# Performance work log

Hardware: AMD Instinct MI355X
Metric: run time of the kernel (lower is better)

Reference implementation:

```python
import jax, jax.numpy as jnp
import numpy as np

EMBED_DIM = 1024
NUM_HEADS = 16
HEAD_DIM = EMBED_DIM // NUM_HEADS


def setup_inputs() -> dict:
    key = jax.random.key(0)
    ks = jax.random.split(key, 6)
    B, S, D = 4, 2048, EMBED_DIM
    scale = 1.0 / np.sqrt(D)
    x = jax.random.normal(ks[0], (B, S, D), dtype=jnp.float32)
    mask = jnp.ones((B, S), dtype=jnp.int32)
    Wq = jax.random.normal(ks[1], (D, D), dtype=jnp.float32) * scale
    Wk = jax.random.normal(ks[2], (D, D), dtype=jnp.float32) * scale
    Wv = jax.random.normal(ks[3], (D, D), dtype=jnp.float32) * scale
    Wo = jax.random.normal(ks[4], (D, D), dtype=jnp.float32) * scale
    bq = jnp.zeros((D,), jnp.float32)
    bk = jnp.zeros((D,), jnp.float32)
    bv = jnp.zeros((D,), jnp.float32)
    bo = jnp.zeros((D,), jnp.float32)
    return {"x": x, "mask": mask, "Wq": Wq, "bq": bq, "Wk": Wk, "bk": bk,
            "Wv": Wv, "bv": bv, "Wo": Wo, "bo": bo}


def reference(x, mask, Wq, bq, Wk, bk, Wv, bv, Wo, bo):
    B, S, D = x.shape
    H, Hd = NUM_HEADS, HEAD_DIM

    def split_heads(t):  # [B,S,D] -> [B,H,S,Hd]
        return t.reshape(B, S, H, Hd).transpose(0, 2, 1, 3)

    q = split_heads(x @ Wq.T + bq)
    k = split_heads(x @ Wk.T + bk)
    v = split_heads(x @ Wv.T + bv)

    scores = jnp.einsum('bhqd,bhkd->bhqk', q, k) / jnp.sqrt(jnp.float32(Hd))
    # mask [B,S] -> broadcast over heads and query positions: [B,1,1,S]
    m = mask[:, None, None, :]
    scores = jnp.where(m == 0, jnp.float32(-1e9), scores)
    attn = jax.nn.softmax(scores, axis=-1)  # dropout_rate=0.0 (eval)
    out = jnp.einsum('bhqk,bhkd->bhqd', attn, v)
    out = out.transpose(0, 2, 1, 3).reshape(B, S, D)
    return out @ Wo.T + bo
```

## Files before the change

### kernel.cpp

```cpp
#include <hip/hip_runtime.h>
#include <stdint.h>

typedef __attribute__((ext_vector_type(8))) short short8;
typedef __attribute__((ext_vector_type(4))) float floatx4;
typedef __attribute__((ext_vector_type(16))) float f32x16;
typedef __attribute__((ext_vector_type(4))) unsigned int uint4v;

#define D_MODEL 1024
#define SEQ     2048
#define NHEAD   16
#define HDIM    64
#define BATCH   4
#define NW      (D_MODEL * D_MODEL)

__device__ __forceinline__ unsigned short f2b(float f) {
  unsigned int u = __builtin_bit_cast(unsigned int, f);
  u += 0x7FFFu + ((u >> 16) & 1u);
  return (unsigned short)(u >> 16);
}

__device__ __forceinline__ floatx4 mfma16(short8 a, short8 b, floatx4 c) {
  return __builtin_amdgcn_mfma_f32_16x16x32_bf16(a, b, c, 0, 0, 0);
}
__device__ __forceinline__ f32x16 mfma32(short8 a, short8 b, f32x16 c) {
  return __builtin_amdgcn_mfma_f32_32x32x16_bf16(a, b, c, 0, 0, 0);
}
__device__ __forceinline__ unsigned int cvtpk(float lo, float hi) {
  unsigned int r;
  asm("v_cvt_pk_bf16_f32 %0, %1, %2" : "=v"(r) : "v"(lo), "v"(hi));
  return r;
}
__device__ __forceinline__ void pl32swap(unsigned int &a, unsigned int &b) {
  asm("v_permlane32_swap_b32 %0, %1" : "+v"(a), "+v"(b));
}
__device__ __forceinline__ float expfast(float x) {
  return __builtin_amdgcn_exp2f(x);
}

#define GLL16(gsrc, ldst)                                                     \
  __builtin_amdgcn_global_load_lds(                                           \
      (const __attribute__((address_space(1))) void*)(gsrc),                  \
      (__attribute__((address_space(3))) void*)(ldst), 16, 0, 0)

__global__ void cvt_f32_bf16(const float* __restrict__ in,
                             unsigned short* __restrict__ out, int n) {
  int idx = (blockIdx.x * blockDim.x + threadIdx.x) * 4;
  int stride = gridDim.x * blockDim.x * 4;
  for (int i = idx; i < n; i += stride) {
    float4 v = *reinterpret_cast<const float4*>(in + i);
    ushort4 o;
    o.x = f2b(v.x); o.y = f2b(v.y); o.z = f2b(v.z); o.w = f2b(v.w);
    *reinterpret_cast<ushort4*>(out + i) = o;
  }
}

__global__ void cvt_w(const float* __restrict__ Wq, const float* __restrict__ Wk,
                      const float* __restrict__ Wv, const float* __restrict__ Wo,
                      unsigned short* __restrict__ Wqkv,
                      unsigned short* __restrict__ Wob,
                      const int* __restrict__ mask, float* __restrict__ maskb) {
  const int which = blockIdx.y;
  int idx = (blockIdx.x * blockDim.x + threadIdx.x) * 4;
  int stride = gridDim.x * blockDim.x * 4;
  if (which == 4) {
    for (int i = idx; i < BATCH * SEQ; i += stride) {
      int4 mv = *reinterpret_cast<const int4*>(mask + i);
      float4 o;
      o.x = mv.x ? 0.f : -1e10f;
      o.y = mv.y ? 0.f : -1e10f;
      o.z = mv.z ? 0.f : -1e10f;
      o.w = mv.w ? 0.f : -1e10f;
      *reinterpret_cast<float4*>(maskb + i) = o;
    }
    return;
  }
  const float* s = which == 0 ? Wq : which == 1 ? Wk : which == 2 ? Wv : Wo;
  unsigned short* d = which < 3 ? Wqkv + (size_t)which * NW : Wob;
  for (int i = idx; i < NW; i += stride) {
    float4 v = *reinterpret_cast<const float4*>(s + i);
    ushort4 o;
    o.x = f2b(v.x); o.y = f2b(v.y); o.z = f2b(v.z); o.w = f2b(v.w);
    *reinterpret_cast<ushort4*>(d + i) = o;
  }
}

__global__ void mask_flags(const int* __restrict__ mask,
                           unsigned int* __restrict__ flags2,
                           const float* __restrict__ bq,
                           const float* __restrict__ bk,
                           const float* __restrict__ bv,
                           float* __restrict__ bqkv) {
  const int b = blockIdx.x, tid = threadIdx.x;
  if (tid < 64) {
    int ok = 0;
    if (tid < 32) {
      ok = 1;
      for (int i = 0; i < 64; ++i) ok &= mask[b * SEQ + tid * 64 + i];
    }
    unsigned long long bal = __ballot(ok);
    if (tid == 0) flags2[b] = (unsigned int)bal;
  }
  const int i = blockIdx.x * 256 + tid;
  bqkv[i] = bq[i];
  bqkv[1024 + i] = bk[i];
  bqkv[2048 + i] = bv[i];
}

template <int MODE>
__global__ __launch_bounds__(256) void gemm_bt(
    const unsigned short* __restrict__ A, const unsigned short* __restrict__ B,
    const float* __restrict__ bias, void* __restrict__ C,
    unsigned short* __restrict__ VT, int M, int N, int K) {
  __shared__ __align__(16) unsigned short As[2][128 * 64];
  __shared__ __align__(16) unsigned short Bs[2][128 * 64];
  const int tid = threadIdx.x;
  const int w = tid >> 6, l = tid & 63, lg = l >> 4, li = l & 15;
  const int GX = (MODE == 1) ? 24 : 8;
  const int NWG = GX * 64;
  int id = blockIdx.y * GX + blockIdx.x;
  id = (id & 7) * (NWG >> 3) + (id >> 3);
  const int m0 = (id / GX) * 128, n0 = (id % GX) * 128;
  const int wr = w >> 1, wc = w & 1;

  floatx4 acc[4][4];
#pragma unroll
  for (int m = 0; m < 4; ++m)
#pragma unroll
    for (int n = 0; n < 4; ++n) acc[m][n] = (floatx4){0.f, 0.f, 0.f, 0.f};

#define GSTAGE(BUF, T)                                                         \
  do {                                                                         \
    _Pragma("unroll") for (int p = 0; p < 4; ++p) {                            \
      const int c = p * 256 + tid;                                             \
      const int row = c >> 3;                                                  \
      const int co = ((c & 7) ^ (row & 7)) * 8;                                \
      GLL16(A + (size_t)(m0 + row) * K + (T) * 64 + co,                        \
            &As[BUF][(p * 256 + w * 64) * 8]);                                 \
      GLL16(B + (size_t)(n0 + row) * K + (T) * 64 + co,                        \
            &Bs[BUF][(p * 256 + w * 64) * 8]);                                 \
    }                                                                          \
  } while (0)

#define GCOMP(BUF)                                                             \
  do {                                                                         \
    _Pragma("unroll") for (int kk = 0; kk < 2; ++kk) {                         \
      short8 af[4], bfr[4];                                                    \
      _Pragma("unroll") for (int m = 0; m < 4; ++m)                            \
        af[m] = *reinterpret_cast<const short8*>(                              \
            &As[BUF][(wr * 64 + m * 16 + li) * 64 +                            \
                     (((kk * 4 + lg) ^ (li & 7)) * 8)]);                       \
      _Pragma("unroll") for (int n = 0; n < 4; ++n)                            \
        bfr[n] = *reinterpret_cast<const short8*>(                             \
            &Bs[BUF][(wc * 64 + n * 16 + li) * 64 +                            \
                     (((kk * 4 + lg) ^ (li & 7)) * 8)]);                       \
      __builtin_amdgcn_s_setprio(1);                                           \
      _Pragma("unroll") for (int m = 0; m < 4; ++m)                            \
        _Pragma("unroll") for (int n = 0; n < 4; ++n)                          \
            acc[m][n] = mfma16(af[m], bfr[n], acc[m][n]);                      \
      __builtin_amdgcn_s_setprio(0);                                           \
    }                                                                          \
  } while (0)

  const int NT = K >> 6;
  GSTAGE(0, 0);
  __syncthreads();
#pragma unroll 1
  for (int t = 0; t < NT; t += 2) {
    if (t + 1 < NT) GSTAGE(1, t + 1);
    GCOMP(0);
    __syncthreads();
    if (t + 2 < NT) GSTAGE(0, t + 2);
    GCOMP(1);
    __syncthreads();
  }
#undef GSTAGE
#undef GCOMP

#pragma unroll
  for (int m = 0; m < 4; ++m)
#pragma unroll
    for (int n = 0; n < 4; ++n) {
      const int gcol = n0 + wc * 64 + n * 16 + li;
      const float bv = bias[gcol];
      const int grow0 = m0 + wr * 64 + m * 16 + lg * 4;
      if (MODE == 1 && n0 >= 2048) {
        const int vc = gcol - 2048;
        const int hh = vc >> 6, dd = vc & 63;
        const int b = grow0 >> 11, s0 = grow0 & 2047;
        ushort4 pk;
        pk.x = f2b(acc[m][n][0] + bv);
        pk.y = f2b(acc[m][n][1] + bv);
        pk.z = f2b(acc[m][n][2] + bv);
        pk.w = f2b(acc[m][n][3] + bv);
        *reinterpret_cast<ushort4*>(
            &VT[((size_t)((b * NHEAD + hh) * HDIM + dd)) * SEQ + s0]) = pk;
      } else {
        const float scl =
            (MODE == 1 && gcol < 1024) ? 0.18033688011112042f : 1.f;
#pragma unroll
        for (int r = 0; r < 4; ++r) {
          const float val = (acc[m][n][r] + bv) * scl;
          if (MODE == 2)
            reinterpret_cast<float*>(C)[(size_t)(grow0 + r) * N + gcol] = val;
          else
            reinterpret_cast<unsigned short*>(C)[(size_t)(grow0 + r) * N + gcol] =
                f2b(val);
        }
      }
    }
}

__global__ __launch_bounds__(512) void attn_v7(
    const unsigned short* __restrict__ QKV, const unsigned short* __restrict__ VT,
    const float* __restrict__ maskb, const unsigned int* __restrict__ flags2,
    unsigned short* __restrict__ O) {
  __shared__ __align__(16) unsigned short Kl[2][64 * 64];
  __shared__ __align__(16) unsigned short Vl[2][64 * 64];
  const int tid = threadIdx.x, w = tid >> 6, l = tid & 63;
  const int qi = l & 31, hi = l >> 5;
  const int bid = blockIdx.x;
  const int qblk = bid >> 6, bh = bid & 63, b = bh >> 4, h = bh & 15;
  const int q0 = qblk * 256 + w * 32;

  const unsigned short* qptr = QKV + (size_t)(b * SEQ + q0 + qi) * 3072 + h * 64;
  short8 qf[4];
#pragma unroll
  for (int ds = 0; ds < 4; ++ds)
    qf[ds] = *reinterpret_cast<const short8*>(qptr + ds * 16 + hi * 8);

  int off[2][4];
#pragma unroll
  for (int kb = 0; kb < 2; ++kb)
#pragma unroll
    for (int ds = 0; ds < 4; ++ds)
      off[kb][ds] = (kb * 32 + qi) * 64 + (((ds * 2 + hi) ^ (qi & 7)) * 8);

  const int srow = tid >> 3;
  const int swz = ((tid & 7) ^ (srow & 7)) * 8;
  const int ldst = w * 512;
  const unsigned short* kp0 =
      QKV + (size_t)(b * SEQ) * 3072 + D_MODEL + h * 64 + (size_t)srow * 3072 + swz;
  const unsigned short* vp0 =
      VT + (size_t)((b * NHEAD + h) * HDIM) * SEQ + (size_t)srow * SEQ + swz;

#define STAGE(BUF)                                                             \
  do {                                                                         \
    GLL16(kp0, &Kl[BUF][ldst]);                                                \
    GLL16(vp0, &Vl[BUF][ldst]);                                                \
    kp0 += 64 * 3072; vp0 += 64;                                               \
  } while (0)

  const float* mrow = maskb + b * SEQ;
  const unsigned int fl = flags2[b];
  f32x16 oa[2] = {};
  float l_run = 0.f;

#define TILE(BUF, KT)                                                          \
  do {                                                                         \
    f32x16 pa0 = {}, pa1 = {};                                                 \
    __builtin_amdgcn_s_setprio(1);                                             \
    _Pragma("unroll") for (int ds = 0; ds < 4; ++ds) {                         \
      const short8 kf0 =                                                       \
          *reinterpret_cast<const short8*>(&Kl[BUF][off[0][ds]]);              \
      const short8 kf1 =                                                       \
          *reinterpret_cast<const short8*>(&Kl[BUF][off[1][ds]]);              \
      pa0 = mfma32(kf0, qf[ds], pa0);                                          \
      pa1 = mfma32(kf1, qf[ds], pa1);                                          \
    }                                                                          \
    __builtin_amdgcn_s_setprio(0);                                             \
    if (!((fl >> (KT)) & 1)) {                \
      _Pragma("unroll") for (int rq = 0; rq < 4; ++rq) {                       \
        const float4 m0 = *reinterpret_cast<const float4*>(                    \
            mrow + (KT) * 64 + rq * 8 + hi * 4);                               \
        const float4 m1 = *reinterpret_cast<const float4*>(                    \
            mrow + (KT) * 64 + 32 + rq * 8 + hi * 4);                          \
        pa0[rq * 4 + 0] += m0.x; pa0[rq * 4 + 1] += m0.y;                      \
        pa0[rq * 4 + 2] += m0.z; pa0[rq * 4 + 3] += m0.w;                      \
        pa1[rq * 4 + 0] += m1.x; pa1[rq * 4 + 1] += m1.y;                      \
        pa1[rq * 4 + 2] += m1.z; pa1[rq * 4 + 3] += m1.w;                      \
      }                                                                        \
    }                                                                          \
    float r0 = 0.f, r1 = 0.f, r2 = 0.f, r3 = 0.f;                              \
    _Pragma("unroll") for (int r = 0; r < 16; r += 4) {                        \
      float p;                                                                 \
      p = expfast(pa0[r + 0]); pa0[r + 0] = p; r0 += p;                        \
      p = expfast(pa0[r + 1]); pa0[r + 1] = p; r1 += p;                        \
      p = expfast(pa0[r + 2]); pa0[r + 2] = p; r2 += p;                        \
      p = expfast(pa0[r + 3]); pa0[r + 3] = p; r3 += p;                        \
      p = expfast(pa1[r + 0]); pa1[r + 0] = p; r0 += p;                        \
      p = expfast(pa1[r + 1]); pa1[r + 1] = p; r1 += p;                        \
      p = expfast(pa1[r + 2]); pa1[r + 2] = p; r2 += p;                        \
      p = expfast(pa1[r + 3]); pa1[r + 3] = p; r3 += p;                        \
    }                                                                          \
    l_run += (r0 + r1) + (r2 + r3);                                            \
    unsigned int c0[8], c1[8];                                                 \
    _Pragma("unroll") for (int u2 = 0; u2 < 8; ++u2) {                         \
      c0[u2] = cvtpk(pa0[2 * u2], pa0[2 * u2 + 1]);                            \
      c1[u2] = cvtpk(pa1[2 * u2], pa1[2 * u2 + 1]);                            \
    }                                                                          \
    pl32swap(c0[0], c0[2]); pl32swap(c0[1], c0[3]);                            \
    pl32swap(c0[4], c0[6]); pl32swap(c0[5], c0[7]);                            \
    pl32swap(c1[0], c1[2]); pl32swap(c1[1], c1[3]);                            \
    pl32swap(c1[4], c1[6]); pl32swap(c1[5], c1[7]);                            \
    __builtin_amdgcn_s_setprio(1);                                             \
    _Pragma("unroll") for (int ks = 0; ks < 4; ++ks) {                         \
      const int kb = ks >> 1, hf = (ks & 1) * 4;                               \
      const short8 pf = __builtin_bit_cast(                                    \
          short8, kb ? (uint4v){c1[hf], c1[hf + 1], c1[hf + 2], c1[hf + 3]}    \
                     : (uint4v){c0[hf], c0[hf + 1], c0[hf + 2], c0[hf + 3]});  \
      const short8 vf0 =                                                       \
          *reinterpret_cast<const short8*>(&Vl[BUF][off[0][ks]]);              \
      const short8 vf1 =                                                       \
          *reinterpret_cast<const short8*>(&Vl[BUF][off[1][ks]]);              \
      oa[0] = mfma32(vf0, pf, oa[0]);                                          \
      oa[1] = mfma32(vf1, pf, oa[1]);                                          \
    }                                                                          \
    __builtin_amdgcn_s_setprio(0);                                             \
  } while (0)

  STAGE(0);
  __syncthreads();
#pragma unroll 1
  for (int kt = 0; kt < 32; kt += 2) {
    STAGE(1);
    TILE(0, kt);
    __syncthreads();
    if (kt + 2 < 32) STAGE(0);
    TILE(1, kt + 1);
    __syncthreads();
  }
#undef STAGE
#undef TILE

  l_run += __shfl_xor(l_run, 32);
  const float rinv = 1.f / l_run;
  unsigned int u[2][8];
#pragma unroll
  for (int vb = 0; vb < 2; ++vb) {
#pragma unroll
    for (int uu = 0; uu < 8; ++uu)
      u[vb][uu] = cvtpk(oa[vb][2 * uu] * rinv, oa[vb][2 * uu + 1] * rinv);
    pl32swap(u[vb][0], u[vb][2]);
    pl32swap(u[vb][1], u[vb][3]);
    pl32swap(u[vb][4], u[vb][6]);
    pl32swap(u[vb][5], u[vb][7]);
  }
  unsigned short* optr = O + (size_t)(b * SEQ + q0 + qi) * D_MODEL + h * 64;
#pragma unroll
  for (int cix = 0; cix < 4; ++cix) {
    const int vb = cix >> 1, hf = (cix & 1) * 4;
    *reinterpret_cast<short8*>(optr + cix * 16 + hi * 8) = __builtin_bit_cast(
        short8,
        (uint4v){u[vb][hf], u[vb][hf + 1], u[vb][hf + 2], u[vb][hf + 3]});
  }
}

extern "C" void kernel_launch(void* const* d_in, const int* in_sizes, int n_in,
                              void* d_out, int out_size, void* d_ws, size_t ws_size,
                              hipStream_t stream) {
  const float* x  = (const float*)d_in[0];
  const int* mask = (const int*)d_in[1];
  const float* Wq = (const float*)d_in[2];
  const float* bq = (const float*)d_in[3];
  const float* Wk = (const float*)d_in[4];
  const float* bk = (const float*)d_in[5];
  const float* Wv = (const float*)d_in[6];
  const float* bv = (const float*)d_in[7];
  const float* Wo = (const float*)d_in[8];
  const float* bo = (const float*)d_in[9];

  char* ws = (char*)d_ws;
  const size_t SZ_X = (size_t)BATCH * SEQ * D_MODEL * 2;
  unsigned short* xb    = (unsigned short*)(ws);
  unsigned short* Wqkvb = (unsigned short*)(ws + SZ_X);
  unsigned short* Wob   = (unsigned short*)(ws + SZ_X + 6u * 1024 * 1024);
  unsigned short* QKVb  = (unsigned short*)(ws + 24u * 1024 * 1024);
  unsigned short* VTb   = (unsigned short*)(ws + 72u * 1024 * 1024);
  float*          bqkv  = (float*)(ws + 88u * 1024 * 1024);
  float*          maskb = (float*)(ws + 88u * 1024 * 1024 + 16384);
  unsigned int*   flag2 = (unsigned int*)(ws + 88u * 1024 * 1024 + 49152);
  unsigned short* Ob    = xb;

  const int NX = BATCH * SEQ * D_MODEL;
  const int M = BATCH * SEQ;

  cvt_f32_bf16<<<2048, 256, 0, stream>>>(x, xb, NX);
  cvt_w<<<dim3(512, 5), 256, 0, stream>>>(Wq, Wk, Wv, Wo, Wqkvb, Wob, mask, maskb);
  mask_flags<<<BATCH, 256, 0, stream>>>(mask, flag2, bq, bk, bv, bqkv);

  gemm_bt<1><<<dim3(3 * D_MODEL / 128, M / 128), 256, 0, stream>>>(
      xb, Wqkvb, bqkv, QKVb, VTb, M, 3 * D_MODEL, D_MODEL);

  attn_v7<<<BATCH * NHEAD * (SEQ / 256), 512, 0, stream>>>(QKVb, VTb, maskb,
                                                           flag2, Ob);

  gemm_bt<2><<<dim3(D_MODEL / 128, M / 128), 256, 0, stream>>>(
      Ob, Wob, bo, d_out, nullptr, M, D_MODEL, D_MODEL);
}
```

Measured before the change: 185.5 us.

## Split attention KV range in two halves with persistent blocks and combine kernel

The attention kernel now splits each (batch, head, query-block) job into two halves over the key/value sequence. 768 persistent blocks loop over 1024 work items, and each writes unnormalized bf16 partial outputs plus row sums to scratch buffers. A new combine kernel adds the two partials and divides by the summed normalizer to produce the attention output. The aim is finer-grained work to improve load balance and CU utilisation, at the cost of an extra kernel launch, extra global traffic for the partials, and slight added rounding from storing the partials in bf16.

```diff
diff --git a/kernel.cpp b/kernel.cpp
--- a/kernel.cpp
+++ b/kernel.cpp
@@ -17,6 +17,9 @@
   unsigned int u = __builtin_bit_cast(unsigned int, f);
   u += 0x7FFFu + ((u >> 16) & 1u);
   return (unsigned short)(u >> 16);
+}
+__device__ __forceinline__ float b2f(unsigned short us) {
+  return __builtin_bit_cast(float, (unsigned int)us << 16);
 }
 
 __device__ __forceinline__ floatx4 mfma16(short8 a, short8 b, floatx4 c) {
@@ -210,149 +213,176 @@
     }
 }
 
-__global__ __launch_bounds__(512) void attn_v7(
+__global__ __launch_bounds__(512) void attn_v8(
     const unsigned short* __restrict__ QKV, const unsigned short* __restrict__ VT,
     const float* __restrict__ maskb, const unsigned int* __restrict__ flags2,
-    unsigned short* __restrict__ O) {
+    unsigned short* __restrict__ OP0, unsigned short* __restrict__ OP1,
+    float* __restrict__ l0g, float* __restrict__ l1g) {
   __shared__ __align__(16) unsigned short Kl[2][64 * 64];
   __shared__ __align__(16) unsigned short Vl[2][64 * 64];
   const int tid = threadIdx.x, w = tid >> 6, l = tid & 63;
   const int qi = l & 31, hi = l >> 5;
-  const int bid = blockIdx.x;
-  const int qblk = bid >> 6, bh = bid & 63, b = bh >> 4, h = bh & 15;
-  const int q0 = qblk * 256 + w * 32;
-
-  const unsigned short* qptr = QKV + (size_t)(b * SEQ + q0 + qi) * 3072 + h * 64;
-  short8 qf[4];
-#pragma unroll
-  for (int ds = 0; ds < 4; ++ds)
-    qf[ds] = *reinterpret_cast<const short8*>(qptr + ds * 16 + hi * 8);
-
-  int off[2][4];
-#pragma unroll
-  for (int kb = 0; kb < 2; ++kb)
+
+#pragma unroll 1
+  for (int item = blockIdx.x; item < 1024; item += 768) {
+    const int bh = item & 63, kvh = (item >> 6) & 1, qblk = item >> 7;
+    const int b = bh >> 4, h = bh & 15;
+    const int q0 = qblk * 256 + w * 32;
+
+    const unsigned short* qptr =
+        QKV + (size_t)(b * SEQ + q0 + qi) * 3072 + h * 64;
+    short8 qf[4];
 #pragma unroll
     for (int ds = 0; ds < 4; ++ds)
-      off[kb][ds] = (kb * 32 + qi) * 64 + (((ds * 2 + hi) ^ (qi & 7)) * 8);
-
-  const int srow = tid >> 3;
-  const int swz = ((tid & 7) ^ (srow & 7)) * 8;
-  const int ldst = w * 512;
-  const unsigned short* kp0 =
-      QKV + (size_t)(b * SEQ) * 3072 + D_MODEL + h * 64 + (size_t)srow * 3072 + swz;
-  const unsigned short* vp0 =
-      VT + (size_t)((b * NHEAD + h) * HDIM) * SEQ + (size_t)srow * SEQ + swz;
-
-#define STAGE(BUF)                                                             \
-  do {                                                                         \
-    GLL16(kp0, &Kl[BUF][ldst]);                                                \
-    GLL16(vp0, &Vl[BUF][ldst]);                                                \
-    kp0 += 64 * 3072; vp0 += 64;                                               \
+      qf[ds] = *reinterpret_cast<const short8*>(qptr + ds * 16 + hi * 8);
+
+    int off[2][4];
+#pragma unroll
+    for (int kb = 0; kb < 2; ++kb)
+#pragma unroll
+      for (int ds = 0; ds < 4; ++ds)
+        off[kb][ds] = (kb * 32 + qi) * 64 + (((ds * 2 + hi) ^ (qi & 7)) * 8);
+
+    const int srow = tid >> 3;
+    const int swz = ((tid & 7) ^ (srow & 7)) * 8;
+    const int ldst = w * 512;
+    const unsigned short* kp0 = QKV + (size_t)(b * SEQ) * 3072 + D_MODEL +
+                                h * 64 +
+                                (size_t)(kvh * 1024 + srow) * 3072 + swz;
+    const unsigned short* vp0 = VT + (size_t)((b * NHEAD + h) * HDIM) * SEQ +
+                                (size_t)srow * SEQ + kvh * 1024 + swz;
+
+#define STAGE(BUF)                                                            \
+  do {                                                                        \
+    GLL16(kp0, &Kl[BUF][ldst]);                                               \
+    GLL16(vp0, &Vl[BUF][ldst]);                                               \
+    kp0 += 64 * 3072; vp0 += 64;                                              \
   } while (0)
 
-  const float* mrow = maskb + b * SEQ;
-  const unsigned int fl = flags2[b];
-  f32x16 oa[2] = {};
-  float l_run = 0.f;
-
-#define TILE(BUF, KT)                                                          \
-  do {                                                                         \
-    f32x16 pa0 = {}, pa1 = {};                                                 \
-    __builtin_amdgcn_s_setprio(1);                                             \
-    _Pragma("unroll") for (int ds = 0; ds < 4; ++ds) {                         \
-      const short8 kf0 =                                                       \
-          *reinterpret_cast<const short8*>(&Kl[BUF][off[0][ds]]);              \
-      const short8 kf1 =                                                       \
-          *reinterpret_cast<const short8*>(&Kl[BUF][off[1][ds]]);              \
-      pa0 = mfma32(kf0, qf[ds], pa0);                                          \
-      pa1 = mfma32(kf1, qf[ds], pa1);                                          \
-    }                                                                          \
-    __builtin_amdgcn_s_setprio(0);                                             \
-    if (!((fl >> (KT)) & 1)) {                \
-      _Pragma("unroll") for (int rq = 0; rq < 4; ++rq) {                       \
-        const float4 m0 = *reinterpret_cast<const float4*>(                    \
-            mrow + (KT) * 64 + rq * 8 + hi * 4);                               \
-        const float4 m1 = *reinterpret_cast<const float4*>(                    \
-            mrow + (KT) * 64 + 32 + rq * 8 + hi * 4);                          \
-        pa0[rq * 4 + 0] += m0.x; pa0[rq * 4 + 1] += m0.y;                      \
-        pa0[rq * 4 + 2] += m0.z; pa0[rq * 4 + 3] += m0.w;                      \
-        pa1[rq * 4 + 0] += m1.x; pa1[rq * 4 + 1] += m1.y;                      \
-        pa1[rq * 4 + 2] += m1.z; pa1[rq * 4 + 3] += m1.w;                      \
-      }                                                                        \
-    }                                                                          \
-    float r0 = 0.f, r1 = 0.f, r2 = 0.f, r3 = 0.f;                              \
-    _Pragma("unroll") for (int r = 0; r < 16; r += 4) {                        \
-      float p;                                                                 \
-      p = expfast(pa0[r + 0]); pa0[r + 0] = p; r0 += p;                        \
-      p = expfast(pa0[r + 1]); pa0[r + 1] = p; r1 += p;                        \
-      p = expfast(pa0[r + 2]); pa0[r + 2] = p; r2 += p;                        \
-      p = expfast(pa0[r + 3]); pa0[r + 3] = p; r3 += p;                        \
-      p = expfast(pa1[r + 0]); pa1[r + 0] = p; r0 += p;                        \
-      p = expfast(pa1[r + 1]); pa1[r + 1] = p; r1 += p;                        \
-      p = expfast(pa1[r + 2]); pa1[r + 2] = p; r2 += p;                        \
-      p = expfast(pa1[r + 3]); pa1[r + 3] = p; r3 += p;                        \
-    }                                                                          \
-    l_run += (r0 + r1) + (r2 + r3);                                            \
-    unsigned int c0[8], c1[8];                                                 \
-    _Pragma("unroll") for (int u2 = 0; u2 < 8; ++u2) {                         \
-      c0[u2] = cvtpk(pa0[2 * u2], pa0[2 * u2 + 1]);                            \
-      c1[u2] = cvtpk(pa1[2 * u2], pa1[2 * u2 + 1]);                            \
-    }                                                                          \
-    pl32swap(c0[0], c0[2]); pl32swap(c0[1], c0[3]);                            \
-    pl32swap(c0[4], c0[6]); pl32swap(c0[5], c0[7]);                            \
-    pl32swap(c1[0], c1[2]); pl32swap(c1[1], c1[3]);                            \
-    pl32swap(c1[4], c1[6]); pl32swap(c1[5], c1[7]);                            \
-    __builtin_amdgcn_s_setprio(1);                                             \
-    _Pragma("unroll") for (int ks = 0; ks < 4; ++ks) {                         \
-      const int kb = ks >> 1, hf = (ks & 1) * 4;                               \
-      const short8 pf = __builtin_bit_cast(                                    \
-          short8, kb ? (uint4v){c1[hf], c1[hf + 1], c1[hf + 2], c1[hf + 3]}    \
-                     : (uint4v){c0[hf], c0[hf + 1], c0[hf + 2], c0[hf + 3]});  \
-      const short8 vf0 =                                                       \
-          *reinterpret_cast<const short8*>(&Vl[BUF][off[0][ks]]);              \
-      const short8 vf1 =                                                       \
-          *reinterpret_cast<const short8*>(&Vl[BUF][off[1][ks]]);              \
-      oa[0] = mfma32(vf0, pf, oa[0]);                                          \
-      oa[1] = mfma32(vf1, pf, oa[1]);                                          \
-    }                                                                          \
-    __builtin_amdgcn_s_setprio(0);                                             \
+    const float* mrow = maskb + b * SEQ;
+    const unsigned int fl = flags2[b];
+    f32x16 oa[2] = {};
+    float l_run = 0.f;
+
+#define TILE(BUF, KT)                                                         \
+  do {                                                                        \
+    f32x16 pa0 = {}, pa1 = {};                                                \
+    __builtin_amdgcn_s_setprio(1);                                            \
+    _Pragma("unroll") for (int ds = 0; ds < 4; ++ds) {                        \
+      const short8 kf0 =                                                      \
+          *reinterpret_cast<const short8*>(&Kl[BUF][off[0][ds]]);             \
+      const short8 kf1 =                                                      \
+          *reinterpret_cast<const short8*>(&Kl[BUF][off[1][ds]]);             \
+      pa0 = mfma32(kf0, qf[ds], pa0);                                         \
+      pa1 = mfma32(kf1, qf[ds], pa1);                                         \
+    }                                                                         \
+    __builtin_amdgcn_s_setprio(0);                                            \
+    if (!((fl >> (KT)) & 1)) {                                                \
+      _Pragma("unroll") for (int rq = 0; rq < 4; ++rq) {                      \
+        const float4 m0 = *reinterpret_cast<const float4*>(                   \
+            mrow + (KT) * 64 + rq * 8 + hi * 4);                              \
+        const float4 m1 = *reinterpret_cast<const float4*>(                   \
+            mrow + (KT) * 64 + 32 + rq * 8 + hi * 4);                         \
+        pa0[rq * 4 + 0] += m0.x; pa0[rq * 4 + 1] += m0.y;                     \
+        pa0[rq * 4 + 2] += m0.z; pa0[rq * 4 + 3] += m0.w;                     \
+        pa1[rq * 4 + 0] += m1.x; pa1[rq * 4 + 1] += m1.y;                     \
+        pa1[rq * 4 + 2] += m1.z; pa1[rq * 4 + 3] += m1.w;                     \
+      }                                                                       \
+    }                                                                         \
+    float r0 = 0.f, r1 = 0.f, r2 = 0.f, r3 = 0.f;                             \
+    _Pragma("unroll") for (int r = 0; r < 16; r += 4) {                       \
+      float p;                                                                \
+      p = expfast(pa0[r + 0]); pa0[r + 0] = p; r0 += p;                       \
+      p = expfast(pa0[r + 1]); pa0[r + 1] = p; r1 += p;                       \
+      p = expfast(pa0[r + 2]); pa0[r + 2] = p; r2 += p;                       \
+      p = expfast(pa0[r + 3]); pa0[r + 3] = p; r3 += p;                       \
+      p = expfast(pa1[r + 0]); pa1[r + 0] = p; r0 += p;                       \
+      p = expfast(pa1[r + 1]); pa1[r + 1] = p; r1 += p;                       \
+      p = expfast(pa1[r + 2]); pa1[r + 2] = p; r2 += p;                       \
+      p = expfast(pa1[r + 3]); pa1[r + 3] = p; r3 += p;                       \
+    }                                                                         \
+    l_run += (r0 + r1) + (r2 + r3);                                           \
+    unsigned int c0[8], c1[8];                                                \
+    _Pragma("unroll") for (int u2 = 0; u2 < 8; ++u2) {                        \
+      c0[u2] = cvtpk(pa0[2 * u2], pa0[2 * u2 + 1]);                           \
+      c1[u2] = cvtpk(pa1[2 * u2], pa1[2 * u2 + 1]);                           \
+    }                                                                         \
+    pl32swap(c0[0], c0[2]); pl32swap(c0[1], c0[3]);                           \
+    pl32swap(c0[4], c0[6]); pl32swap(c0[5], c0[7]);                           \
+    pl32swap(c1[0], c1[2]); pl32swap(c1[1], c1[3]);                           \
+    pl32swap(c1[4], c1[6]); pl32swap(c1[5], c1[7]);                           \
+    __builtin_amdgcn_s_setprio(1);                                            \
+    _Pragma("unroll") for (int ks = 0; ks < 4; ++ks) {                        \
+      const int kb = ks >> 1, hf = (ks & 1) * 4;                              \
+      const short8 pf = __builtin_bit_cast(                                   \
+          short8, kb ? (uint4v){c1[hf], c1[hf + 1], c1[hf + 2], c1[hf + 3]}   \
+                     : (uint4v){c0[hf], c0[hf + 1], c0[hf + 2], c0[hf + 3]}); \
+      const short8 vf0 =                                                      \
+          *reinterpret_cast<const short8*>(&Vl[BUF][off[0][ks]]);             \
+      const short8 vf1 =                                                      \
+          *reinterpret_cast<const short8*>(&Vl[BUF][off[1][ks]]);             \
+      oa[0] = mfma32(vf0, pf, oa[0]);                                         \
+      oa[1] = mfma32(vf1, pf, oa[1]);                                         \
+    }                                                                         \
+    __builtin_amdgcn_s_setprio(0);                                            \
   } while (0)
 
-  STAGE(0);
-  __syncthreads();
+    const int ktEnd = kvh * 16 + 16;
+    STAGE(0);
+    __syncthreads();
 #pragma unroll 1
-  for (int kt = 0; kt < 32; kt += 2) {
-    STAGE(1);
-    TILE(0, kt);
-    __syncthreads();
-    if (kt + 2 < 32) STAGE(0);
-    TILE(1, kt + 1);
-    __syncthreads();
-  }
+    for (int kt = kvh * 16; kt < ktEnd; kt += 2) {
+      STAGE(1);
+      TILE(0, kt);
+      __syncthreads();
+      if (kt + 2 < ktEnd) STAGE(0);
+      TILE(1, kt + 1);
+      __syncthreads();
+    }
 #undef STAGE
 #undef TILE
 
-  l_run += __shfl_xor(l_run, 32);
-  const float rinv = 1.f / l_run;
-  unsigned int u[2][8];
-#pragma unroll
-  for (int vb = 0; vb < 2; ++vb) {
-#pragma unroll
-    for (int uu = 0; uu < 8; ++uu)
-      u[vb][uu] = cvtpk(oa[vb][2 * uu] * rinv, oa[vb][2 * uu + 1] * rinv);
-    pl32swap(u[vb][0], u[vb][2]);
-    pl32swap(u[vb][1], u[vb][3]);
-    pl32swap(u[vb][4], u[vb][6]);
-    pl32swap(u[vb][5], u[vb][7]);
-  }
-  unsigned short* optr = O + (size_t)(b * SEQ + q0 + qi) * D_MODEL + h * 64;
-#pragma unroll
-  for (int cix = 0; cix < 4; ++cix) {
-    const int vb = cix >> 1, hf = (cix & 1) * 4;
-    *reinterpret_cast<short8*>(optr + cix * 16 + hi * 8) = __builtin_bit_cast(
-        short8,
-        (uint4v){u[vb][hf], u[vb][hf + 1], u[vb][hf + 2], u[vb][hf + 3]});
-  }
+    l_run += __shfl_xor(l_run, 32);
+    unsigned int u[2][8];
+#pragma unroll
+    for (int vb = 0; vb < 2; ++vb) {
+#pragma unroll
+      for (int uu = 0; uu < 8; ++uu)
+        u[vb][uu] = cvtpk(oa[vb][2 * uu], oa[vb][2 * uu + 1]);
+      pl32swap(u[vb][0], u[vb][2]);
+      pl32swap(u[vb][1], u[vb][3]);
+      pl32swap(u[vb][4], u[vb][6]);
+      pl32swap(u[vb][5], u[vb][7]);
+    }
+    const size_t qrow = (size_t)(b * SEQ) + q0 + qi;
+    if (hi == 0) (kvh ? l1g : l0g)[qrow * NHEAD + h] = l_run;
+    unsigned short* op = kvh ? OP1 + qrow * 3072 + 2048 + h * 64
+                             : OP0 + qrow * 1024 + h * 64;
+#pragma unroll
+    for (int cix = 0; cix < 4; ++cix) {
+      const int vb = cix >> 1, hf = (cix & 1) * 4;
+      *reinterpret_cast<short8*>(op + cix * 16 + hi * 8) = __builtin_bit_cast(
+          short8,
+          (uint4v){u[vb][hf], u[vb][hf + 1], u[vb][hf + 2], u[vb][hf + 3]});
+    }
+  }
+}
+
+__global__ void combine(const unsigned short* __restrict__ OP0,
+                        const unsigned short* __restrict__ OP1,
+                        const float* __restrict__ l0g,
+                        const float* __restrict__ l1g,
+                        unsigned short* __restrict__ Ob) {
+  const int i8 = (blockIdx.x * 256 + threadIdx.x) * 8;
+  const int q = i8 >> 10, hd = i8 & 1023, h = hd >> 6;
+  const float r = 1.f / (l0g[q * NHEAD + h] + l1g[q * NHEAD + h]);
+  short8 a = *reinterpret_cast<const short8*>(OP0 + i8);
+  short8 c = *reinterpret_cast<const short8*>(OP1 + (size_t)q * 3072 + 2048 + hd);
+  short8 o;
+#pragma unroll
+  for (int j = 0; j < 8; ++j)
+    o[j] = (short)f2b((b2f((unsigned short)a[j]) + b2f((unsigned short)c[j])) * r);
+  *reinterpret_cast<short8*>(Ob + i8) = o;
 }
 
 extern "C" void kernel_launch(void* const* d_in, const int* in_sizes, int n_in,
@@ -376,10 +406,15 @@
   unsigned short* Wob   = (unsigned short*)(ws + SZ_X + 6u * 1024 * 1024);
   unsigned short* QKVb  = (unsigned short*)(ws + 24u * 1024 * 1024);
   unsigned short* VTb   = (unsigned short*)(ws + 72u * 1024 * 1024);
-  float*          bqkv  = (float*)(ws + 88u * 1024 * 1024);
-  float*          maskb = (float*)(ws + 88u * 1024 * 1024 + 16384);
-  unsigned int*   flag2 = (unsigned int*)(ws + 88u * 1024 * 1024 + 49152);
-  unsigned short* Ob    = xb;
+  char*           aux   = ws + 88u * 1024 * 1024;
+  float*          bqkv  = (float*)(aux);
+  float*          maskb = (float*)(aux + 16384);
+  unsigned int*   flag2 = (unsigned int*)(aux + 49152);
+  float*          l0g   = (float*)(aux + 65536);
+  float*          l1g   = (float*)(aux + 65536 + 524288);
+  unsigned short* OP0   = xb;
+  unsigned short* OP1   = QKVb;
+  unsigned short* Ob    = VTb;
 
   const int NX = BATCH * SEQ * D_MODEL;
   const int M = BATCH * SEQ;
@@ -391,8 +426,9 @@
   gemm_bt<1><<<dim3(3 * D_MODEL / 128, M / 128), 256, 0, stream>>>(
       xb, Wqkvb, bqkv, QKVb, VTb, M, 3 * D_MODEL, D_MODEL);
 
-  attn_v7<<<BATCH * NHEAD * (SEQ / 256), 512, 0, stream>>>(QKVb, VTb, maskb,
-                                                           flag2, Ob);
+  attn_v8<<<768, 512, 0, stream>>>(QKVb, VTb, maskb, flag2, OP0, OP1, l0g, l1g);
+
+  combine<<<4096, 256, 0, stream>>>(OP0, OP1, l0g, l1g, Ob);
 
   gemm_bt<2><<<dim3(D_MODEL / 128, M / 128), 256, 0, stream>>>(
       Ob, Wob, bo, d_out, nullptr, M, D_MODEL, D_MODEL);
```

New measurement: 198.4 us. 1.07x slower.

## Process two 32-row query tiles per wave in attention to reuse K/V loads

Applied to the files above, without the earlier changes.

Each wave in the attention kernel now handles 64 query rows (two 32-row sub-tiles) instead of 32, so every K and V fragment read from LDS feeds twice as many MFMAs. Each block covers 512 queries, and the grid shrinks from 512 to 256 blocks. This halves per-query K/V global and LDS traffic and barrier overhead. The cost is roughly double the accumulator registers, which can lower occupancy, and a grid of 256 blocks may underfill the GPU's compute units.

```diff
diff --git a/kernel.cpp b/kernel.cpp
--- a/kernel.cpp
+++ b/kernel.cpp
@@ -210,7 +210,7 @@
     }
 }
 
-__global__ __launch_bounds__(512) void attn_v7(
+__global__ __launch_bounds__(512) void attn_v9(
     const unsigned short* __restrict__ QKV, const unsigned short* __restrict__ VT,
     const float* __restrict__ maskb, const unsigned int* __restrict__ flags2,
     unsigned short* __restrict__ O) {
@@ -220,13 +220,19 @@
   const int qi = l & 31, hi = l >> 5;
   const int bid = blockIdx.x;
   const int qblk = bid >> 6, bh = bid & 63, b = bh >> 4, h = bh & 15;
-  const int q0 = qblk * 256 + w * 32;
-
-  const unsigned short* qptr = QKV + (size_t)(b * SEQ + q0 + qi) * 3072 + h * 64;
-  short8 qf[4];
-#pragma unroll
-  for (int ds = 0; ds < 4; ++ds)
-    qf[ds] = *reinterpret_cast<const short8*>(qptr + ds * 16 + hi * 8);
+  const int q0 = qblk * 512 + w * 64;
+
+  short8 qf0[4], qf1[4];
+  {
+    const unsigned short* qp0 =
+        QKV + (size_t)(b * SEQ + q0 + qi) * 3072 + h * 64;
+    const unsigned short* qp1 = qp0 + (size_t)32 * 3072;
+#pragma unroll
+    for (int ds = 0; ds < 4; ++ds) {
+      qf0[ds] = *reinterpret_cast<const short8*>(qp0 + ds * 16 + hi * 8);
+      qf1[ds] = *reinterpret_cast<const short8*>(qp1 + ds * 16 + hi * 8);
+    }
+  }
 
   int off[2][4];
 #pragma unroll
@@ -252,20 +258,39 @@
 
   const float* mrow = maskb + b * SEQ;
   const unsigned int fl = flags2[b];
-  f32x16 oa[2] = {};
-  float l_run = 0.f;
+  f32x16 oa00 = {}, oa01 = {}, oa10 = {}, oa11 = {};
+  float lr0 = 0.f, lr1 = 0.f;
+
+#define EXPPACK(PA, C, LR)                                                     \
+  do {                                                                         \
+    float r0 = 0.f, r1 = 0.f, r2 = 0.f, r3 = 0.f;                              \
+    _Pragma("unroll") for (int r = 0; r < 16; r += 4) {                        \
+      float p;                                                                 \
+      p = expfast(PA[r + 0]); PA[r + 0] = p; r0 += p;                          \
+      p = expfast(PA[r + 1]); PA[r + 1] = p; r1 += p;                          \
+      p = expfast(PA[r + 2]); PA[r + 2] = p; r2 += p;                          \
+      p = expfast(PA[r + 3]); PA[r + 3] = p; r3 += p;                          \
+    }                                                                          \
+    LR += (r0 + r1) + (r2 + r3);                                               \
+    _Pragma("unroll") for (int u2 = 0; u2 < 8; ++u2)                           \
+        C[u2] = cvtpk(PA[2 * u2], PA[2 * u2 + 1]);                             \
+    pl32swap(C[0], C[2]); pl32swap(C[1], C[3]);                                \
+    pl32swap(C[4], C[6]); pl32swap(C[5], C[7]);                                \
+  } while (0)
 
 #define TILE(BUF, KT)                                                          \
   do {                                                                         \
-    f32x16 pa0 = {}, pa1 = {};                                                 \
+    f32x16 pa00 = {}, pa01 = {}, pa10 = {}, pa11 = {};                         \
     __builtin_amdgcn_s_setprio(1);                                             \
     _Pragma("unroll") for (int ds = 0; ds < 4; ++ds) {                         \
       const short8 kf0 =                                                       \
           *reinterpret_cast<const short8*>(&Kl[BUF][off[0][ds]]);              \
       const short8 kf1 =                                                       \
           *reinterpret_cast<const short8*>(&Kl[BUF][off[1][ds]]);              \
-      pa0 = mfma32(kf0, qf[ds], pa0);                                          \
-      pa1 = mfma32(kf1, qf[ds], pa1);                                          \
+      pa00 = mfma32(kf0, qf0[ds], pa00);                                       \
+      pa01 = mfma32(kf1, qf0[ds], pa01);                                       \
+      pa10 = mfma32(kf0, qf1[ds], pa10);                                       \
+      pa11 = mfma32(kf1, qf1[ds], pa11);                                       \
     }                                                                          \
     __builtin_amdgcn_s_setprio(0);                                             \
     if (!((fl >> (KT)) & 1)) {                \
@@ -274,46 +299,40 @@
             mrow + (KT) * 64 + rq * 8 + hi * 4);                               \
         const float4 m1 = *reinterpret_cast<const float4*>(                    \
             mrow + (KT) * 64 + 32 + rq * 8 + hi * 4);                          \
-        pa0[rq * 4 + 0] += m0.x; pa0[rq * 4 + 1] += m0.y;                      \
-        pa0[rq * 4 + 2] += m0.z; pa0[rq * 4 + 3] += m0.w;                      \
-        pa1[rq * 4 + 0] += m1.x; pa1[rq * 4 + 1] += m1.y;                      \
-        pa1[rq * 4 + 2] += m1.z; pa1[rq * 4 + 3] += m1.w;                      \
+        pa00[rq * 4 + 0] += m0.x; pa00[rq * 4 + 1] += m0.y;                    \
+        pa00[rq * 4 + 2] += m0.z; pa00[rq * 4 + 3] += m0.w;                    \
+        pa01[rq * 4 + 0] += m1.x; pa01[rq * 4 + 1] += m1.y;                    \
+        pa01[rq * 4 + 2] += m1.z; pa01[rq * 4 + 3] += m1.w;                    \
+        pa10[rq * 4 + 0] += m0.x; pa10[rq * 4 + 1] += m0.y;                    \
+        pa10[rq * 4 + 2] += m0.z; pa10[rq * 4 + 3] += m0.w;                    \
+        pa11[rq * 4 + 0] += m1.x; pa11[rq * 4 + 1] += m1.y;                    \
+        pa11[rq * 4 + 2] += m1.z; pa11[rq * 4 + 3] += m1.w;                    \
       }                                                                        \
     }                                                                          \
-    float r0 = 0.f, r1 = 0.f, r2 = 0.f, r3 = 0.f;                              \
-    _Pragma("unroll") for (int r = 0; r < 16; r += 4) {                        \
-      float p;                                                                 \
-      p = expfast(pa0[r + 0]); pa0[r + 0] = p; r0 += p;                        \
-      p = expfast(pa0[r + 1]); pa0[r + 1] = p; r1 += p;                        \
-      p = expfast(pa0[r + 2]); pa0[r + 2] = p; r2 += p;                        \
-      p = expfast(pa0[r + 3]); pa0[r + 3] = p; r3 += p;                        \
-      p = expfast(pa1[r + 0]); pa1[r + 0] = p; r0 += p;                        \
-      p = expfast(pa1[r + 1]); pa1[r + 1] = p; r1 += p;                        \
-      p = expfast(pa1[r + 2]); pa1[r + 2] = p; r2 += p;                        \
-      p = expfast(pa1[r + 3]); pa1[r + 3] = p; r3 += p;                        \
-    }                                                                          \
-    l_run += (r0 + r1) + (r2 + r3);                                            \
-    unsigned int c0[8], c1[8];                                                 \
-    _Pragma("unroll") for (int u2 = 0; u2 < 8; ++u2) {                         \
-      c0[u2] = cvtpk(pa0[2 * u2], pa0[2 * u2 + 1]);                            \
-      c1[u2] = cvtpk(pa1[2 * u2], pa1[2 * u2 + 1]);                            \
-    }                                                                          \
-    pl32swap(c0[0], c0[2]); pl32swap(c0[1], c0[3]);                            \
-    pl32swap(c0[4], c0[6]); pl32swap(c0[5], c0[7]);                            \
-    pl32swap(c1[0], c1[2]); pl32swap(c1[1], c1[3]);                            \
-    pl32swap(c1[4], c1[6]); pl32swap(c1[5], c1[7]);                            \
+    unsigned int c00[8], c01[8], c10[8], c11[8];                               \
+    EXPPACK(pa00, c00, lr0);                                                   \
+    EXPPACK(pa01, c01, lr0);                                                   \
+    EXPPACK(pa10, c10, lr1);                                                   \
+    EXPPACK(pa11, c11, lr1);                                                   \
     __builtin_amdgcn_s_setprio(1);                                             \
     _Pragma("unroll") for (int ks = 0; ks < 4; ++ks) {                         \
-      const int kb = ks >> 1, hf = (ks & 1) * 4;                               \
-      const short8 pf = __builtin_bit_cast(                                    \
-          short8, kb ? (uint4v){c1[hf], c1[hf + 1], c1[hf + 2], c1[hf + 3]}    \
-                     : (uint4v){c0[hf], c0[hf + 1], c0[hf + 2], c0[hf + 3]});  \
+      const int hf = (ks & 1) * 4;                                             \
       const short8 vf0 =                                                       \
           *reinterpret_cast<const short8*>(&Vl[BUF][off[0][ks]]);              \
       const short8 vf1 =                                                       \
           *reinterpret_cast<const short8*>(&Vl[BUF][off[1][ks]]);              \
-      oa[0] = mfma32(vf0, pf, oa[0]);                                          \
-      oa[1] = mfma32(vf1, pf, oa[1]);                                          \
+      const short8 pf0 = __builtin_bit_cast(                                   \
+          short8,                                                              \
+          (ks >> 1) ? (uint4v){c01[hf], c01[hf + 1], c01[hf + 2], c01[hf + 3]} \
+                    : (uint4v){c00[hf], c00[hf + 1], c00[hf + 2], c00[hf + 3]}); \
+      const short8 pf1 = __builtin_bit_cast(                                   \
+          short8,                                                              \
+          (ks >> 1) ? (uint4v){c11[hf], c11[hf + 1], c11[hf + 2], c11[hf + 3]} \
+                    : (uint4v){c10[hf], c10[hf + 1], c10[hf + 2], c10[hf + 3]}); \
+      oa00 = mfma32(vf0, pf0, oa00);                                           \
+      oa01 = mfma32(vf1, pf0, oa01);                                           \
+      oa10 = mfma32(vf0, pf1, oa10);                                           \
+      oa11 = mfma32(vf1, pf1, oa11);                                           \
     }                                                                          \
     __builtin_amdgcn_s_setprio(0);                                             \
   } while (0)
@@ -331,28 +350,37 @@
   }
 #undef STAGE
 #undef TILE
-
-  l_run += __shfl_xor(l_run, 32);
-  const float rinv = 1.f / l_run;
-  unsigned int u[2][8];
-#pragma unroll
-  for (int vb = 0; vb < 2; ++vb) {
-#pragma unroll
-    for (int uu = 0; uu < 8; ++uu)
-      u[vb][uu] = cvtpk(oa[vb][2 * uu] * rinv, oa[vb][2 * uu + 1] * rinv);
-    pl32swap(u[vb][0], u[vb][2]);
-    pl32swap(u[vb][1], u[vb][3]);
-    pl32swap(u[vb][4], u[vb][6]);
-    pl32swap(u[vb][5], u[vb][7]);
-  }
-  unsigned short* optr = O + (size_t)(b * SEQ + q0 + qi) * D_MODEL + h * 64;
-#pragma unroll
-  for (int cix = 0; cix < 4; ++cix) {
-    const int vb = cix >> 1, hf = (cix & 1) * 4;
-    *reinterpret_cast<short8*>(optr + cix * 16 + hi * 8) = __builtin_bit_cast(
-        short8,
-        (uint4v){u[vb][hf], u[vb][hf + 1], u[vb][hf + 2], u[vb][hf + 3]});
-  }
+#undef EXPPACK
+
+#define EPI(OA0, OA1, LR, QOFF)                                                \
+  do {                                                                         \
+    LR += __shfl_xor(LR, 32);                                                  \
+    const float rinv = 1.f / LR;                                               \
+    unsigned int u0[8], u1[8];                                                 \
+    _Pragma("unroll") for (int uu = 0; uu < 8; ++uu) {                         \
+      u0[uu] = cvtpk(OA0[2 * uu] * rinv, OA0[2 * uu + 1] * rinv);              \
+      u1[uu] = cvtpk(OA1[2 * uu] * rinv, OA1[2 * uu + 1] * rinv);              \
+    }                                                                          \
+    pl32swap(u0[0], u0[2]); pl32swap(u0[1], u0[3]);                            \
+    pl32swap(u0[4], u0[6]); pl32swap(u0[5], u0[7]);                            \
+    pl32swap(u1[0], u1[2]); pl32swap(u1[1], u1[3]);                            \
+    pl32swap(u1[4], u1[6]); pl32swap(u1[5], u1[7]);                            \
+    unsigned short* optr =                                                     \
+        O + (size_t)(b * SEQ + q0 + (QOFF) + qi) * D_MODEL + h * 64;           \
+    _Pragma("unroll") for (int cix = 0; cix < 4; ++cix) {                      \
+      const int hf = (cix & 1) * 4;                                            \
+      *reinterpret_cast<short8*>(optr + cix * 16 + hi * 8) =                   \
+          __builtin_bit_cast(                                                  \
+              short8,                                                          \
+              (cix >> 1)                                                       \
+                  ? (uint4v){u1[hf], u1[hf + 1], u1[hf + 2], u1[hf + 3]}       \
+                  : (uint4v){u0[hf], u0[hf + 1], u0[hf + 2], u0[hf + 3]});     \
+    }                                                                          \
+  } while (0)
+
+  EPI(oa00, oa01, lr0, 0);
+  EPI(oa10, oa11, lr1, 32);
+#undef EPI
 }
 
 extern "C" void kernel_launch(void* const* d_in, const int* in_sizes, int n_in,
@@ -391,7 +419,7 @@
   gemm_bt<1><<<dim3(3 * D_MODEL / 128, M / 128), 256, 0, stream>>>(
       xb, Wqkvb, bqkv, QKVb, VTb, M, 3 * D_MODEL, D_MODEL);
 
-  attn_v7<<<BATCH * NHEAD * (SEQ / 256), 512, 0, stream>>>(QKVb, VTb, maskb,
+  attn_v9<<<BATCH * NHEAD * (SEQ / 512), 512, 0, stream>>>(QKVb, VTb, maskb,
                                                            flag2, Ob);
 
   gemm_bt<2><<<dim3(D_MODEL / 128, M / 128), 256, 0, stream>>>(
```

Result: slower. 192.8 us (+3.9%).
